# Performance work log

Hardware: AMD Instinct MI355X
Metric: run time of the kernel (lower is better)

The kernel has to match this reference:

```python
import jax, jax.numpy as jnp
import numpy as np

TOP_K = 2
NORM_TOPK_PROB = True


def setup_inputs() -> dict:
    key = jax.random.key(0)
    k1, k2, k3, k4 = jax.random.split(key, 4)
    B, S, H = 1, 1024, 2048
    E, I = 16, 768
    hidden_states = jax.random.normal(k1, (B, S, H), dtype=jnp.float32)
    # 0.02 init scale keeps router logits / activations in a realistic range
    gate_w = jax.random.normal(k2, (E, H), dtype=jnp.float32) * 0.02
    w1 = jax.random.normal(k3, (E, 2 * I, H), dtype=jnp.float32) * 0.02  # [gate; up] stacked
    w2 = jax.random.normal(k4, (E, H, I), dtype=jnp.float32) * 0.02
    return {"hidden_states": hidden_states, "gate_w": gate_w, "w1": w1, "w2": w2}


def reference(hidden_states, gate_w, w1, w2):
    B, S, H = hidden_states.shape
    E = gate_w.shape[0]
    I = w2.shape[2]
    x = hidden_states.reshape(-1, H)  # [T, H]

    # Router
    router_logits = x @ gate_w.T  # [T, E]
    probs = jax.nn.softmax(router_logits.astype(jnp.float32), axis=-1)
    topk_w, topk_ids = jax.lax.top_k(probs, TOP_K)  # [T, K]
    if NORM_TOPK_PROB:
        topk_w = topk_w / jnp.sum(topk_w, axis=-1, keepdims=True)
    topk_w = topk_w.astype(x.dtype)

    # combine[t, e] = sum_k topk_w[t, k] * 1[topk_ids[t, k] == e]
    combine = jnp.sum(jax.nn.one_hot(topk_ids, E, dtype=x.dtype) * topk_w[..., None], axis=1)  # [T, E]

    def expert(w1_e, w2_e):
        h = x @ w1_e.T                      # [T, 2I]
        act = jax.nn.silu(h[:, :I]) * h[:, I:]  # fused SiLU-and-mul
        return act @ w2_e.T                 # [T, H]

    y_all = jax.vmap(expert)(w1, w2)        # [E, T, H]
    out = jnp.einsum('te,eth->th', combine, y_all)  # weighted scatter-sum over experts
    return out, router_logits
```

## Files before the change

kernel.cpp:

```cpp
#include <hip/hip_runtime.h>
#include <hip/hip_bf16.h>


#define T_TOK 1024
#define HDIM  2048
#define NEXP  16
#define IDIM  768
#define CAP   192

typedef __attribute__((ext_vector_type(8))) short  short8_t;
typedef __attribute__((ext_vector_type(4))) float  f32x4_t;

static __device__ __forceinline__ unsigned short f2bf(float f) {
  unsigned u = __float_as_uint(f);
  u += 0x7FFFu + ((u >> 16) & 1u);
  return (unsigned short)(u >> 16);
}
static __device__ __forceinline__ short f2bf_t(float f) {
  return (short)(__float_as_uint(f) >> 16);
}
static __device__ __forceinline__ float bf2f(unsigned short h) {
  return __uint_as_float(((unsigned)h) << 16);
}
static __device__ __forceinline__ void cvt_store4(unsigned short* dst, float4 v) {
  ushort4 u;
  u.x = f2bf(v.x); u.y = f2bf(v.y); u.z = f2bf(v.z); u.w = f2bf(v.w);
  *(ushort4*)dst = u;
}
static __device__ __forceinline__ short8_t pack_bf16(float4 lo, float4 hi) {
  short8_t r;
  r[0] = f2bf_t(lo.x); r[1] = f2bf_t(lo.y); r[2] = f2bf_t(lo.z); r[3] = f2bf_t(lo.w);
  r[4] = f2bf_t(hi.x); r[5] = f2bf_t(hi.y); r[6] = f2bf_t(hi.z); r[7] = f2bf_t(hi.w);
  return r;
}
static __device__ __forceinline__ void gl2lds16(const void* g, void* l) {
  __builtin_amdgcn_global_load_lds(
      (const __attribute__((address_space(1))) unsigned int*)g,
      (__attribute__((address_space(3))) unsigned int*)l, 16, 0, 0);
}

__global__ __launch_bounds__(256) void cvt_x(
    const float* __restrict__ x, unsigned short* __restrict__ xb) {
  int i = blockIdx.x * 256 + threadIdx.x;
  float4 v = ((const float4*)x)[i];
  cvt_store4(xb + (size_t)i * 4, v);
}

__global__ __launch_bounds__(256) void moe_router(
    const float* __restrict__ x, const float* __restrict__ gw,
    float* __restrict__ logits_out, int* __restrict__ cnt,
    int* __restrict__ tok, float* __restrict__ wl) {
  const int t = blockIdx.x;
  const int tid = threadIdx.x;
  const int lane = tid & 63, wid = tid >> 6;
  const float4* xv = (const float4*)(x + (size_t)t * HDIM);
  float4 v0 = xv[tid * 2], v1 = xv[tid * 2 + 1];
  float acc[NEXP];
#pragma unroll
  for (int e = 0; e < NEXP; ++e) {
    const float4* gv = (const float4*)(gw + (size_t)e * HDIM);
    float4 g0 = gv[tid * 2], g1 = gv[tid * 2 + 1];
    acc[e] = v0.x * g0.x + v0.y * g0.y + v0.z * g0.z + v0.w * g0.w +
             v1.x * g1.x + v1.y * g1.y + v1.z * g1.z + v1.w * g1.w;
  }
#pragma unroll
  for (int e = 0; e < NEXP; ++e)
#pragma unroll
    for (int off = 32; off; off >>= 1) acc[e] += __shfl_xor(acc[e], off, 64);
  __shared__ float red[4][NEXP];
  if (lane == 0)
#pragma unroll
    for (int e = 0; e < NEXP; ++e) red[wid][e] = acc[e];
  __syncthreads();
  if (tid < NEXP) {
    float s = red[0][tid] + red[1][tid] + red[2][tid] + red[3][tid];
    logits_out[(size_t)t * NEXP + tid] = s;
    red[0][tid] = s;
  }
  __syncthreads();
  if (tid == 0) {
    int e1 = -1, e2 = -1;
    float l1 = -1e30f, l2 = -1e30f;
#pragma unroll
    for (int e = 0; e < NEXP; ++e) {
      float v = red[0][e];
      if (v > l1)      { l2 = l1; e2 = e1; l1 = v; e1 = e; }
      else if (v > l2) { l2 = v;  e2 = e; }
    }
    float wa = 1.f / (1.f + __expf(l2 - l1));
    float wb = 1.f - wa;
    int p1 = atomicAdd(&cnt[e1], 1);
    if (p1 < CAP) { tok[e1 * CAP + p1] = t; wl[e1 * CAP + p1] = wa; }
    int p2 = atomicAdd(&cnt[e2], 1);
    if (p2 < CAP) { tok[e2 * CAP + p2] = t; wl[e2 * CAP + p2] = wb; }
  }
}

__global__ __launch_bounds__(256) void moe_stage_a(
    const unsigned short* __restrict__ xb, const float* __restrict__ w1,
    const int* __restrict__ cnt, const int* __restrict__ tok,
    unsigned short* __restrict__ h_ws) {
  int bx = blockIdx.x;
  const int ks = bx & 1;
  const int nt = (bx >> 1) % 24;
  const int e  = (bx >> 1) / 24;
  int ne = cnt[e]; if (ne > CAP) ne = CAP;

  __shared__ unsigned short As[192 * 32];
  __shared__ float          Bs[64 * 32];
  __shared__ int toksL[192];
  const int tid = threadIdx.x;
  if (tid < 192) toksL[tid] = tok[e * CAP + (tid < ne ? tid : ne - 1)];
  __syncthreads();

  const int w = tid >> 6, lane = tid & 63;
  const int k0 = ks * 1024;

  const unsigned short* aG[3];
  unsigned short* aL[3];
#pragma unroll
  for (int jj = 0; jj < 3; ++jj) {
    int j = w * 3 + jj;
    int row = 16 * j + (lane >> 2);
    aG[jj] = xb + (size_t)toksL[row] * HDIM + k0 + (lane & 3) * 8;
    aL[jj] = As + j * 512;
  }
  const float* bG[2];
  float* bL[2];
#pragma unroll
  for (int jj = 0; jj < 2; ++jj) {
    int j = w * 2 + jj;
    int nrow = 8 * j + (lane >> 3);
    int d = ((lane & 7) - (lane >> 3)) & 7;
    bG[jj] = w1 + ((size_t)e * (2 * IDIM) + nt * 64 + nrow) * HDIM + k0 + d * 4;
    bL[jj] = Bs + j * 256;
  }

  const int quad = lane >> 4, lr = lane & 15;
  f32x4_t acc[3][4] = {};

  for (int kk = 0; kk < 1024; kk += 32) {
#pragma unroll
    for (int jj = 0; jj < 3; ++jj) gl2lds16(aG[jj] + kk, aL[jj]);
#pragma unroll
    for (int jj = 0; jj < 2; ++jj) gl2lds16(bG[jj] + kk, bL[jj]);
    __syncthreads();

    short8_t a[3], b[4];
#pragma unroll
    for (int mf = 0; mf < 3; ++mf) {
      int row = w * 48 + mf * 16 + lr;
      a[mf] = *(const short8_t*)&As[row * 32 + quad * 8];
    }
#pragma unroll
    for (int nf = 0; nf < 4; ++nf) {
      int r = nf * 16 + lr;
      int p0 = (2 * quad + r) & 7, p1 = (2 * quad + 1 + r) & 7;
      float4 f0 = *(const float4*)&Bs[r * 32 + p0 * 4];
      float4 f1 = *(const float4*)&Bs[r * 32 + p1 * 4];
      b[nf] = pack_bf16(f0, f1);
    }
#pragma unroll
    for (int mf = 0; mf < 3; ++mf)
#pragma unroll
      for (int nf = 0; nf < 4; ++nf)
        acc[mf][nf] = __builtin_amdgcn_mfma_f32_16x16x32_bf16(
            a[mf], b[nf], acc[mf][nf], 0, 0, 0);
    __syncthreads();
  }

  unsigned short* hp = h_ws + ((size_t)ks * NEXP + e) * CAP * (2 * IDIM);
#pragma unroll
  for (int mf = 0; mf < 3; ++mf) {
#pragma unroll
    for (int rr = 0; rr < 4; ++rr) {
      int mg = w * 48 + mf * 16 + quad * 4 + rr;
#pragma unroll
      for (int nf = 0; nf < 4; ++nf) {
        int ng = nt * 64 + nf * 16 + lr;
        hp[(size_t)mg * (2 * IDIM) + ng] = f2bf(acc[mf][nf][rr]);
      }
    }
  }
}

__global__ __launch_bounds__(256) void moe_merge(
    const unsigned short* __restrict__ h_ws, unsigned short* __restrict__ act) {
  const size_t part = (size_t)NEXP * CAP * (2 * IDIM);
  int c = blockIdx.x * 256 + threadIdx.x;
  int row = c / (IDIM / 4);
  int c4  = c % (IDIM / 4);
  size_t gb = (size_t)row * (2 * IDIM) + c4 * 4;
  ushort4 g0 = *(const ushort4*)(h_ws + gb);
  ushort4 g1 = *(const ushort4*)(h_ws + part + gb);
  ushort4 u0 = *(const ushort4*)(h_ws + gb + IDIM);
  ushort4 u1 = *(const ushort4*)(h_ws + part + gb + IDIM);
  float g, u; ushort4 o;
  g = bf2f(g0.x) + bf2f(g1.x); u = bf2f(u0.x) + bf2f(u1.x);
  o.x = f2bf(g / (1.f + __expf(-g)) * u);
  g = bf2f(g0.y) + bf2f(g1.y); u = bf2f(u0.y) + bf2f(u1.y);
  o.y = f2bf(g / (1.f + __expf(-g)) * u);
  g = bf2f(g0.z) + bf2f(g1.z); u = bf2f(u0.z) + bf2f(u1.z);
  o.z = f2bf(g / (1.f + __expf(-g)) * u);
  g = bf2f(g0.w) + bf2f(g1.w); u = bf2f(u0.w) + bf2f(u1.w);
  o.w = f2bf(g / (1.f + __expf(-g)) * u);
  *(ushort4*)(act + (size_t)row * IDIM + c4 * 4) = o;
}

__global__ __launch_bounds__(256) void moe_stage_b(
    const unsigned short* __restrict__ act, const float* __restrict__ w2,
    const int* __restrict__ cnt, const int* __restrict__ tok,
    const float* __restrict__ wl, float* __restrict__ out) {
  int bx = blockIdx.x;
  const int ks = bx & 1;
  const int nt = (bx >> 1) & 31;
  const int e  = bx >> 6;
  int ne = cnt[e]; if (ne > CAP) ne = CAP;

  __shared__ unsigned short As[192 * 32];
  __shared__ float          Bs[64 * 32];
  __shared__ int   toksL[192];
  __shared__ float wtsL[192];
  const int tid = threadIdx.x;
  if (tid < 192) {
    bool v = tid < ne;
    toksL[tid] = tok[e * CAP + (v ? tid : ne - 1)];
    wtsL[tid]  = v ? wl[e * CAP + tid] : 0.f;
  }
  __syncthreads();

  const int w = tid >> 6, lane = tid & 63;
  const int k0 = ks * 384;

  const unsigned short* aG[3];
  unsigned short* aL[3];
#pragma unroll
  for (int jj = 0; jj < 3; ++jj) {
    int j = w * 3 + jj;
    int slot = 16 * j + (lane >> 2);
    aG[jj] = act + ((size_t)e * CAP + slot) * IDIM + k0 + (lane & 3) * 8;
    aL[jj] = As + j * 512;
  }
  const float* bG[2];
  float* bL[2];
#pragma unroll
  for (int jj = 0; jj < 2; ++jj) {
    int j = w * 2 + jj;
    int nrow = 8 * j + (lane >> 3);
    int d = ((lane & 7) - (lane >> 3)) & 7;
    bG[jj] = w2 + ((size_t)e * HDIM + nt * 64 + nrow) * IDIM + k0 + d * 4;
    bL[jj] = Bs + j * 256;
  }

  const int quad = lane >> 4, lr = lane & 15;
  f32x4_t acc[3][4] = {};

  for (int kk = 0; kk < 384; kk += 32) {
#pragma unroll
    for (int jj = 0; jj < 3; ++jj) gl2lds16(aG[jj] + kk, aL[jj]);
#pragma unroll
    for (int jj = 0; jj < 2; ++jj) gl2lds16(bG[jj] + kk, bL[jj]);
    __syncthreads();

    short8_t a[3], b[4];
#pragma unroll
    for (int mf = 0; mf < 3; ++mf) {
      int row = w * 48 + mf * 16 + lr;
      a[mf] = *(const short8_t*)&As[row * 32 + quad * 8];
    }
#pragma unroll
    for (int nf = 0; nf < 4; ++nf) {
      int r = nf * 16 + lr;
      int p0 = (2 * quad + r) & 7, p1 = (2 * quad + 1 + r) & 7;
      float4 f0 = *(const float4*)&Bs[r * 32 + p0 * 4];
      float4 f1 = *(const float4*)&Bs[r * 32 + p1 * 4];
      b[nf] = pack_bf16(f0, f1);
    }
#pragma unroll
    for (int mf = 0; mf < 3; ++mf)
#pragma unroll
      for (int nf = 0; nf < 4; ++nf)
        acc[mf][nf] = __builtin_amdgcn_mfma_f32_16x16x32_bf16(
            a[mf], b[nf], acc[mf][nf], 0, 0, 0);
    __syncthreads();
  }

#pragma unroll
  for (int mf = 0; mf < 3; ++mf) {
#pragma unroll
    for (int rr = 0; rr < 4; ++rr) {
      int sl = w * 48 + mf * 16 + quad * 4 + rr;
      if (sl < ne) {
        float wgt = wtsL[sl];
        int   t   = toksL[sl];
#pragma unroll
        for (int nf = 0; nf < 4; ++nf) {
          int ng = nt * 64 + nf * 16 + lr;
          atomicAdd(&out[(size_t)t * HDIM + ng], acc[mf][nf][rr] * wgt);
        }
      }
    }
  }
}

extern "C" void kernel_launch(void* const* d_in, const int* in_sizes, int n_in,
                              void* d_out, int out_size, void* d_ws,
                              size_t ws_size, hipStream_t stream) {
  (void)in_sizes; (void)n_in; (void)out_size; (void)ws_size;
  const float* x  = (const float*)d_in[0];
  const float* gw = (const float*)d_in[1];
  const float* w1 = (const float*)d_in[2];
  const float* w2 = (const float*)d_in[3];
  float* out    = (float*)d_out;
  float* logits = out + (size_t)T_TOK * HDIM;

  char* ws = (char*)d_ws;
  int*   cnt = (int*)ws;
  int*   tok = (int*)(ws + 256);
  float* wl  = (float*)(ws + 256 + NEXP * CAP * 4);
  unsigned short* xb  = (unsigned short*)(ws + 24832);
  unsigned short* act = xb;
  unsigned short* h_ws =
      (unsigned short*)(ws + 24832 + (size_t)NEXP * CAP * IDIM * 2);

  hipMemsetAsync(cnt, 0, 256, stream);
  hipMemsetAsync(d_out, 0, (size_t)T_TOK * HDIM * sizeof(float), stream);

  cvt_x      <<<T_TOK * HDIM / 4 / 256, 256, 0, stream>>>(x, xb);
  moe_router <<<T_TOK, 256, 0, stream>>>(x, gw, logits, cnt, tok, wl);
  moe_stage_a<<<NEXP * 24 * 2, 256, 0, stream>>>(xb, w1, cnt, tok, h_ws);
  moe_merge  <<<NEXP * CAP * IDIM / 4 / 256, 256, 0, stream>>>(h_ws, act);
  moe_stage_b<<<NEXP * 32 * 2, 256, 0, stream>>>(act, w2, cnt, tok, wl, out);
}
```

Measured before the change: 445.7 us.

## Double-buffer GEMM stages, fuse x conversion into router, replace atomics with combine

Result: faster. 430.6 us (-3.4%).

```diff
diff --git a/kernel.cpp b/kernel.cpp
--- a/kernel.cpp
+++ b/kernel.cpp
@@ -22,39 +22,37 @@
 static __device__ __forceinline__ float bf2f(unsigned short h) {
   return __uint_as_float(((unsigned)h) << 16);
 }
-static __device__ __forceinline__ void cvt_store4(unsigned short* dst, float4 v) {
-  ushort4 u;
-  u.x = f2bf(v.x); u.y = f2bf(v.y); u.z = f2bf(v.z); u.w = f2bf(v.w);
-  *(ushort4*)dst = u;
-}
 static __device__ __forceinline__ short8_t pack_bf16(float4 lo, float4 hi) {
   short8_t r;
   r[0] = f2bf_t(lo.x); r[1] = f2bf_t(lo.y); r[2] = f2bf_t(lo.z); r[3] = f2bf_t(lo.w);
   r[4] = f2bf_t(hi.x); r[5] = f2bf_t(hi.y); r[6] = f2bf_t(hi.z); r[7] = f2bf_t(hi.w);
   return r;
 }
+static __device__ __forceinline__ short8_t pack8_rne(float4 lo, float4 hi) {
+  short8_t r;
+  r[0] = (short)f2bf(lo.x); r[1] = (short)f2bf(lo.y);
+  r[2] = (short)f2bf(lo.z); r[3] = (short)f2bf(lo.w);
+  r[4] = (short)f2bf(hi.x); r[5] = (short)f2bf(hi.y);
+  r[6] = (short)f2bf(hi.z); r[7] = (short)f2bf(hi.w);
+  return r;
+}
 static __device__ __forceinline__ void gl2lds16(const void* g, void* l) {
   __builtin_amdgcn_global_load_lds(
       (const __attribute__((address_space(1))) unsigned int*)g,
       (__attribute__((address_space(3))) unsigned int*)l, 16, 0, 0);
 }
 
-__global__ __launch_bounds__(256) void cvt_x(
-    const float* __restrict__ x, unsigned short* __restrict__ xb) {
-  int i = blockIdx.x * 256 + threadIdx.x;
-  float4 v = ((const float4*)x)[i];
-  cvt_store4(xb + (size_t)i * 4, v);
-}
-
 __global__ __launch_bounds__(256) void moe_router(
     const float* __restrict__ x, const float* __restrict__ gw,
     float* __restrict__ logits_out, int* __restrict__ cnt,
-    int* __restrict__ tok, float* __restrict__ wl) {
+    int* __restrict__ tok, int* __restrict__ inv, float* __restrict__ invw,
+    unsigned short* __restrict__ xb) {
   const int t = blockIdx.x;
   const int tid = threadIdx.x;
   const int lane = tid & 63, wid = tid >> 6;
   const float4* xv = (const float4*)(x + (size_t)t * HDIM);
   float4 v0 = xv[tid * 2], v1 = xv[tid * 2 + 1];
+  *(short8_t*)(xb + (size_t)t * HDIM + tid * 8) = pack8_rne(v0, v1);
   float acc[NEXP];
 #pragma unroll
   for (int e = 0; e < NEXP; ++e) {
@@ -90,9 +88,13 @@
     float wa = 1.f / (1.f + __expf(l2 - l1));
     float wb = 1.f - wa;
     int p1 = atomicAdd(&cnt[e1], 1);
-    if (p1 < CAP) { tok[e1 * CAP + p1] = t; wl[e1 * CAP + p1] = wa; }
+    int i0 = 0; float w0 = 0.f;
+    if (p1 < CAP) { tok[e1 * CAP + p1] = t; i0 = e1 * CAP + p1; w0 = wa; }
+    inv[t * 2] = i0; invw[t * 2] = w0;
     int p2 = atomicAdd(&cnt[e2], 1);
-    if (p2 < CAP) { tok[e2 * CAP + p2] = t; wl[e2 * CAP + p2] = wb; }
+    int i1 = 0; float w1 = 0.f;
+    if (p2 < CAP) { tok[e2 * CAP + p2] = t; i1 = e2 * CAP + p2; w1 = wb; }
+    inv[t * 2 + 1] = i1; invw[t * 2 + 1] = w1;
   }
 }
 
@@ -101,63 +103,78 @@
     const int* __restrict__ cnt, const int* __restrict__ tok,
     unsigned short* __restrict__ h_ws) {
   int bx = blockIdx.x;
+  bx = (bx & 7) * 96 + (bx >> 3);
   const int ks = bx & 1;
   const int nt = (bx >> 1) % 24;
   const int e  = (bx >> 1) / 24;
   int ne = cnt[e]; if (ne > CAP) ne = CAP;
 
-  __shared__ unsigned short As[192 * 32];
-  __shared__ float          Bs[64 * 32];
+  __shared__ unsigned short As[2][192 * 32];
+  __shared__ float          Bs[2][64 * 32];
   __shared__ int toksL[192];
   const int tid = threadIdx.x;
-  if (tid < 192) toksL[tid] = tok[e * CAP + (tid < ne ? tid : ne - 1)];
+  if (tid < 192)
+    toksL[tid] = tok[e * CAP + (tid < ne ? tid : (ne ? ne - 1 : 0))] & (T_TOK - 1);
   __syncthreads();
 
   const int w = tid >> 6, lane = tid & 63;
   const int k0 = ks * 1024;
 
   const unsigned short* aG[3];
-  unsigned short* aL[3];
+  int aOff[3];
 #pragma unroll
   for (int jj = 0; jj < 3; ++jj) {
     int j = w * 3 + jj;
     int row = 16 * j + (lane >> 2);
     aG[jj] = xb + (size_t)toksL[row] * HDIM + k0 + (lane & 3) * 8;
-    aL[jj] = As + j * 512;
+    aOff[jj] = j * 512;
   }
   const float* bG[2];
-  float* bL[2];
+  int bOff[2];
 #pragma unroll
   for (int jj = 0; jj < 2; ++jj) {
     int j = w * 2 + jj;
     int nrow = 8 * j + (lane >> 3);
     int d = ((lane & 7) - (lane >> 3)) & 7;
     bG[jj] = w1 + ((size_t)e * (2 * IDIM) + nt * 64 + nrow) * HDIM + k0 + d * 4;
-    bL[jj] = Bs + j * 256;
+    bOff[jj] = j * 256;
   }
 
   const int quad = lane >> 4, lr = lane & 15;
   f32x4_t acc[3][4] = {};
 
-  for (int kk = 0; kk < 1024; kk += 32) {
-#pragma unroll
-    for (int jj = 0; jj < 3; ++jj) gl2lds16(aG[jj] + kk, aL[jj]);
-#pragma unroll
-    for (int jj = 0; jj < 2; ++jj) gl2lds16(bG[jj] + kk, bL[jj]);
-    __syncthreads();
+#pragma unroll
+  for (int jj = 0; jj < 3; ++jj) gl2lds16(aG[jj], &As[0][aOff[jj]]);
+#pragma unroll
+  for (int jj = 0; jj < 2; ++jj) gl2lds16(bG[jj], &Bs[0][bOff[jj]]);
+
+  for (int it = 0; it < 32; ++it) {
+    const int cur = it & 1;
+    if (it < 31) {
+      const int kk = (it + 1) * 32;
+#pragma unroll
+      for (int jj = 0; jj < 3; ++jj) gl2lds16(aG[jj] + kk, &As[cur ^ 1][aOff[jj]]);
+#pragma unroll
+      for (int jj = 0; jj < 2; ++jj) gl2lds16(bG[jj] + kk, &Bs[cur ^ 1][bOff[jj]]);
+      asm volatile("s_waitcnt vmcnt(5)" ::: "memory");
+    } else {
+      asm volatile("s_waitcnt vmcnt(0)" ::: "memory");
+    }
+    __builtin_amdgcn_s_barrier();
+    __builtin_amdgcn_sched_barrier(0);
 
     short8_t a[3], b[4];
 #pragma unroll
     for (int mf = 0; mf < 3; ++mf) {
       int row = w * 48 + mf * 16 + lr;
-      a[mf] = *(const short8_t*)&As[row * 32 + quad * 8];
+      a[mf] = *(const short8_t*)&As[cur][row * 32 + quad * 8];
     }
 #pragma unroll
     for (int nf = 0; nf < 4; ++nf) {
       int r = nf * 16 + lr;
       int p0 = (2 * quad + r) & 7, p1 = (2 * quad + 1 + r) & 7;
-      float4 f0 = *(const float4*)&Bs[r * 32 + p0 * 4];
-      float4 f1 = *(const float4*)&Bs[r * 32 + p1 * 4];
+      float4 f0 = *(const float4*)&Bs[cur][r * 32 + p0 * 4];
+      float4 f1 = *(const float4*)&Bs[cur][r * 32 + p1 * 4];
       b[nf] = pack_bf16(f0, f1);
     }
 #pragma unroll
@@ -166,7 +183,9 @@
       for (int nf = 0; nf < 4; ++nf)
         acc[mf][nf] = __builtin_amdgcn_mfma_f32_16x16x32_bf16(
             a[mf], b[nf], acc[mf][nf], 0, 0, 0);
-    __syncthreads();
+    asm volatile("s_waitcnt lgkmcnt(0)" ::: "memory");
+    __builtin_amdgcn_s_barrier();
+    __builtin_amdgcn_sched_barrier(0);
   }
 
   unsigned short* hp = h_ws + ((size_t)ks * NEXP + e) * CAP * (2 * IDIM);
@@ -209,71 +228,72 @@
 
 __global__ __launch_bounds__(256) void moe_stage_b(
     const unsigned short* __restrict__ act, const float* __restrict__ w2,
-    const int* __restrict__ cnt, const int* __restrict__ tok,
-    const float* __restrict__ wl, float* __restrict__ out) {
+    float* __restrict__ y) {
   int bx = blockIdx.x;
-  const int ks = bx & 1;
-  const int nt = (bx >> 1) & 31;
-  const int e  = bx >> 6;
-  int ne = cnt[e]; if (ne > CAP) ne = CAP;
-
-  __shared__ unsigned short As[192 * 32];
-  __shared__ float          Bs[64 * 32];
-  __shared__ int   toksL[192];
-  __shared__ float wtsL[192];
+  bx = (bx & 7) * 64 + (bx >> 3);
+  const int nt = bx & 31;
+  const int e  = bx >> 5;
+
+  __shared__ unsigned short As[2][192 * 32];
+  __shared__ float          Bs[2][64 * 32];
   const int tid = threadIdx.x;
-  if (tid < 192) {
-    bool v = tid < ne;
-    toksL[tid] = tok[e * CAP + (v ? tid : ne - 1)];
-    wtsL[tid]  = v ? wl[e * CAP + tid] : 0.f;
-  }
-  __syncthreads();
-
   const int w = tid >> 6, lane = tid & 63;
-  const int k0 = ks * 384;
 
   const unsigned short* aG[3];
-  unsigned short* aL[3];
+  int aOff[3];
 #pragma unroll
   for (int jj = 0; jj < 3; ++jj) {
     int j = w * 3 + jj;
     int slot = 16 * j + (lane >> 2);
-    aG[jj] = act + ((size_t)e * CAP + slot) * IDIM + k0 + (lane & 3) * 8;
-    aL[jj] = As + j * 512;
+    aG[jj] = act + ((size_t)e * CAP + slot) * IDIM + (lane & 3) * 8;
+    aOff[jj] = j * 512;
   }
   const float* bG[2];
-  float* bL[2];
+  int bOff[2];
 #pragma unroll
   for (int jj = 0; jj < 2; ++jj) {
     int j = w * 2 + jj;
     int nrow = 8 * j + (lane >> 3);
     int d = ((lane & 7) - (lane >> 3)) & 7;
-    bG[jj] = w2 + ((size_t)e * HDIM + nt * 64 + nrow) * IDIM + k0 + d * 4;
-    bL[jj] = Bs + j * 256;
+    bG[jj] = w2 + ((size_t)e * HDIM + nt * 64 + nrow) * IDIM + d * 4;
+    bOff[jj] = j * 256;
   }
 
   const int quad = lane >> 4, lr = lane & 15;
   f32x4_t acc[3][4] = {};
 
-  for (int kk = 0; kk < 384; kk += 32) {
-#pragma unroll
-    for (int jj = 0; jj < 3; ++jj) gl2lds16(aG[jj] + kk, aL[jj]);
-#pragma unroll
-    for (int jj = 0; jj < 2; ++jj) gl2lds16(bG[jj] + kk, bL[jj]);
-    __syncthreads();
+#pragma unroll
+  for (int jj = 0; jj < 3; ++jj) gl2lds16(aG[jj], &As[0][aOff[jj]]);
+#pragma unroll
+  for (int jj = 0; jj < 2; ++jj) gl2lds16(bG[jj], &Bs[0][bOff[jj]]);
+
+  for (int it = 0; it < 24; ++it) {
+    const int cur = it & 1;
+    if (it < 23) {
+      const int kk = (it + 1) * 32;
+#pragma unroll
+      for (int jj = 0; jj < 3; ++jj) gl2lds16(aG[jj] + kk, &As[cur ^ 1][aOff[jj]]);
+#pragma unroll
+      for (int jj = 0; jj < 2; ++jj) gl2lds16(bG[jj] + kk, &Bs[cur ^ 1][bOff[jj]]);
+      asm volatile("s_waitcnt vmcnt(5)" ::: "memory");
+    } else {
+      asm volatile("s_waitcnt vmcnt(0)" ::: "memory");
+    }
+    __builtin_amdgcn_s_barrier();
+    __builtin_amdgcn_sched_barrier(0);
 
     short8_t a[3], b[4];
 #pragma unroll
     for (int mf = 0; mf < 3; ++mf) {
       int row = w * 48 + mf * 16 + lr;
-      a[mf] = *(const short8_t*)&As[row * 32 + quad * 8];
+      a[mf] = *(const short8_t*)&As[cur][row * 32 + quad * 8];
     }
 #pragma unroll
     for (int nf = 0; nf < 4; ++nf) {
       int r = nf * 16 + lr;
       int p0 = (2 * quad + r) & 7, p1 = (2 * quad + 1 + r) & 7;
-      float4 f0 = *(const float4*)&Bs[r * 32 + p0 * 4];
-      float4 f1 = *(const float4*)&Bs[r * 32 + p1 * 4];
+      float4 f0 = *(const float4*)&Bs[cur][r * 32 + p0 * 4];
+      float4 f1 = *(const float4*)&Bs[cur][r * 32 + p1 * 4];
       b[nf] = pack_bf16(f0, f1);
     }
 #pragma unroll
@@ -282,7 +302,9 @@
       for (int nf = 0; nf < 4; ++nf)
         acc[mf][nf] = __builtin_amdgcn_mfma_f32_16x16x32_bf16(
             a[mf], b[nf], acc[mf][nf], 0, 0, 0);
-    __syncthreads();
+    asm volatile("s_waitcnt lgkmcnt(0)" ::: "memory");
+    __builtin_amdgcn_s_barrier();
+    __builtin_amdgcn_sched_barrier(0);
   }
 
 #pragma unroll
@@ -290,16 +312,34 @@
 #pragma unroll
     for (int rr = 0; rr < 4; ++rr) {
       int sl = w * 48 + mf * 16 + quad * 4 + rr;
-      if (sl < ne) {
-        float wgt = wtsL[sl];
-        int   t   = toksL[sl];
-#pragma unroll
-        for (int nf = 0; nf < 4; ++nf) {
-          int ng = nt * 64 + nf * 16 + lr;
-          atomicAdd(&out[(size_t)t * HDIM + ng], acc[mf][nf][rr] * wgt);
-        }
+#pragma unroll
+      for (int nf = 0; nf < 4; ++nf) {
+        int ng = nt * 64 + nf * 16 + lr;
+        y[((size_t)e * CAP + sl) * HDIM + ng] = acc[mf][nf][rr];
       }
     }
+  }
+}
+
+__global__ __launch_bounds__(256) void moe_combine(
+    const float* __restrict__ y, const int* __restrict__ inv,
+    const float* __restrict__ invw, float* __restrict__ out) {
+  const int t = blockIdx.x;
+  const int i0 = inv[t * 2], i1 = inv[t * 2 + 1];
+  const float w0 = invw[t * 2], w1 = invw[t * 2 + 1];
+  const float4* y0 = (const float4*)(y + (size_t)i0 * HDIM);
+  const float4* y1 = (const float4*)(y + (size_t)i1 * HDIM);
+  float4* op = (float4*)(out + (size_t)t * HDIM);
+#pragma unroll
+  for (int rep = 0; rep < 2; ++rep) {
+    int c = threadIdx.x + rep * 256;
+    float4 a = y0[c], b = y1[c];
+    float4 r;
+    r.x = w0 * a.x + w1 * b.x;
+    r.y = w0 * a.y + w1 * b.y;
+    r.z = w0 * a.z + w1 * b.z;
+    r.w = w0 * a.w + w1 * b.w;
+    op[c] = r;
   }
 }
 
@@ -315,20 +355,20 @@
   float* logits = out + (size_t)T_TOK * HDIM;
 
   char* ws = (char*)d_ws;
-  int*   cnt = (int*)ws;
-  int*   tok = (int*)(ws + 256);
-  float* wl  = (float*)(ws + 256 + NEXP * CAP * 4);
-  unsigned short* xb  = (unsigned short*)(ws + 24832);
+  int*   cnt  = (int*)ws;
+  int*   tok  = (int*)(ws + 256);
+  int*   inv  = (int*)(ws + 12544);
+  float* invw = (float*)(ws + 20736);
+  unsigned short* xb  = (unsigned short*)(ws + 28928);
   unsigned short* act = xb;
-  unsigned short* h_ws =
-      (unsigned short*)(ws + 24832 + (size_t)NEXP * CAP * IDIM * 2);
+  unsigned short* h_ws = (unsigned short*)(ws + 4747520);
+  float*          yb   = (float*)(ws + 23621888);
 
   hipMemsetAsync(cnt, 0, 256, stream);
-  hipMemsetAsync(d_out, 0, (size_t)T_TOK * HDIM * sizeof(float), stream);
-
-  cvt_x      <<<T_TOK * HDIM / 4 / 256, 256, 0, stream>>>(x, xb);
-  moe_router <<<T_TOK, 256, 0, stream>>>(x, gw, logits, cnt, tok, wl);
+
+  moe_router <<<T_TOK, 256, 0, stream>>>(x, gw, logits, cnt, tok, inv, invw, xb);
   moe_stage_a<<<NEXP * 24 * 2, 256, 0, stream>>>(xb, w1, cnt, tok, h_ws);
   moe_merge  <<<NEXP * CAP * IDIM / 4 / 256, 256, 0, stream>>>(h_ws, act);
-  moe_stage_b<<<NEXP * 32 * 2, 256, 0, stream>>>(act, w2, cnt, tok, wl, out);
-}
+  moe_stage_b<<<NEXP * 32, 256, 0, stream>>>(act, w2, yb);
+  moe_combine<<<T_TOK, 256, 0, stream>>>(yb, inv, invw, out);
+}
```
